# Kernel tuning notes

Measured on AMD Instinct MI355X. Metric: run time of the kernel, lower is better.

The kernel has to match this reference:

```python
import jax, jax.numpy as jnp
import numpy as np

N_QUBITS = 10
DIM = 2 ** N_QUBITS
N_TOKENS = 32
LAYERS = 2
DEGREE = 3
VOCAB = 32000
EMB = 512
N_PARAMS = 4 * N_QUBITS * LAYERS      # angles per token circuit
N_PARAMS_FF = 4 * N_QUBITS            # quantum feedforward (1 layer)
BATCH = 32


def _ry(state, wire, theta, n):
    # state: [B, 2**n] complex64; theta: [B] float32. RY = [[c,-s],[s,c]], c=cos(th/2)
    st = state.reshape(-1, 2 ** wire, 2, 2 ** (n - wire - 1))
    c = jnp.cos(theta / 2)[:, None, None]
    s = jnp.sin(theta / 2)[:, None, None]
    a, b = st[:, :, 0, :], st[:, :, 1, :]
    st = jnp.stack([c * a - s * b, s * a + c * b], axis=2)
    return st.reshape(-1, 2 ** n)


def _crx(state, ctrl, tgt, theta, n):
    # controlled-RX: apply RX=[[c,-i s],[-i s,c]] on tgt where ctrl bit == 1
    lo, hi = (ctrl, tgt) if ctrl < tgt else (tgt, ctrl)
    st = state.reshape(-1, 2 ** lo, 2, 2 ** (hi - lo - 1), 2, 2 ** (n - hi - 1))
    caxis = 2 if ctrl < tgt else 4
    taxis = 4 if ctrl < tgt else 2
    c = jnp.cos(theta / 2).reshape(-1, 1, 1, 1, 1, 1)
    s = jnp.sin(theta / 2).reshape(-1, 1, 1, 1, 1, 1)
    c0 = jax.lax.index_in_dim(st, 0, caxis, keepdims=True)
    c1 = jax.lax.index_in_dim(st, 1, caxis, keepdims=True)
    a = jax.lax.index_in_dim(c1, 0, taxis, keepdims=True)
    b = jax.lax.index_in_dim(c1, 1, taxis, keepdims=True)
    na = c * a - 1j * s * b
    nb = -1j * s * a + c * b
    c1 = jnp.concatenate([na, nb], axis=taxis)
    st = jnp.concatenate([c0, c1], axis=caxis)
    return st.reshape(-1, 2 ** n)


def _ansatz14(state, params, n, layers):
    # gate order of ansatz 14 (arXiv:1905.10876); params: [B, 4*n*layers]
    idx = 0
    for _ in range(layers):
        for i in range(n):
            state = _ry(state, i, params[:, idx], n); idx += 1
        for i in range(n - 1, -1, -1):
            state = _crx(state, i, (i + 1) % n, params[:, idx], n); idx += 1
        for i in range(n):
            state = _ry(state, i, params[:, idx], n); idx += 1
        for i in [n - 1] + list(range(n - 1)):
            state = _crx(state, i, (i - 1) % n, params[:, idx], n); idx += 1
    return state


def _measure_xyz(state, n):
    # expectation of X,Y,Z on every wire; output [B, 3*n] ordered [x..., y..., z...]
    B = state.shape[0]
    xs, ys, zs = [], [], []
    for w in range(n):
        st = state.reshape(B, 2 ** w, 2, 2 ** (n - w - 1))
        a, b = st[:, :, 0, :], st[:, :, 1, :]
        z = jnp.sum(jnp.conj(a) * b, axis=(1, 2))
        xs.append(2.0 * jnp.real(z))
        ys.append(2.0 * jnp.imag(z))
        zs.append(jnp.sum(jnp.real(a * jnp.conj(a)) - jnp.real(b * jnp.conj(b)), axis=(1, 2)))
    return jnp.stack(xs + ys + zs, axis=1)


def _forward(x, emb, w_ang, b_ang, qsvt_coeffs, lcu_re, lcu_im, qff_params, w1, b1, w2, b2):
    B, T = x.shape
    lcu = (lcu_re + 1j * lcu_im).astype(jnp.complex64)
    lcu = lcu / jnp.maximum(jnp.sum(jnp.abs(lcu)), 1e-12)          # p=1 normalize
    angles = (emb[x] @ w_ang.T + b_ang).reshape(B * T, N_PARAMS)   # [B*T, P]
    init = jnp.zeros((B, DIM), jnp.complex64).at[:, 0].set(1.0)
    acc = qsvt_coeffs[0] * init
    mono = init
    for k in range(1, DEGREE + 1):
        rep = jnp.repeat(mono, T, axis=0)                          # [B*T, D]
        st = _ansatz14(rep, angles, N_QUBITS, LAYERS).reshape(B, T, DIM)
        mono = jnp.einsum('bwi,w->bi', st, lcu)                    # LCU combine
        acc = acc + qsvt_coeffs[k] * mono
    qsvt_state = acc / jnp.sum(jnp.abs(qsvt_coeffs))
    norm = jnp.linalg.norm(qsvt_state, axis=-1, keepdims=True)
    normed = qsvt_state / jnp.maximum(norm, 1e-12)
    qff = jnp.broadcast_to(qff_params[None, :], (B, N_PARAMS_FF))
    st2 = _ansatz14(normed, qff, N_QUBITS, 1)
    ev = _measure_xyz(st2, N_QUBITS)                               # [B, 3*nq]
    h = jax.nn.relu(ev @ w1.T + b1)
    logits = h @ w2.T + b2
    return logits, jnp.mean(norm[:, 0])


def setup_inputs() -> dict:
    key = jax.random.key(0)
    ks = jax.random.split(key, 9)
    return {
        'x': jax.random.randint(ks[0], (BATCH, N_TOKENS), 0, VOCAB, dtype=jnp.int32),
        'emb': jax.random.normal(ks[1], (VOCAB, EMB), jnp.float32) * 0.02,
        'w_ang': jax.random.normal(ks[2], (N_PARAMS, EMB), jnp.float32) * (1.0 / np.sqrt(EMB)),
        'b_ang': jnp.zeros((N_PARAMS,), jnp.float32),
        'qsvt_coeffs': jax.random.uniform(ks[3], (DEGREE + 1,), jnp.float32),
        'lcu_re': jax.random.uniform(ks[4], (N_TOKENS,), jnp.float32),
        'lcu_im': jax.random.uniform(ks[5], (N_TOKENS,), jnp.float32),
        'qff_params': jax.random.uniform(ks[6], (N_PARAMS_FF,), jnp.float32),
        'w1': jax.random.normal(ks[7], (EMB, 3 * N_QUBITS), jnp.float32) * (1.0 / np.sqrt(3 * N_QUBITS)),
        'b1': jnp.zeros((EMB,), jnp.float32),
        'w2': jax.random.normal(ks[8], (VOCAB, EMB), jnp.float32) * (1.0 / np.sqrt(EMB)),
        'b2': jnp.zeros((VOCAB,), jnp.float32),
    }


def reference(x, emb, w_ang, b_ang, qsvt_coeffs, lcu_re, lcu_im, qff_params, w1, b1, w2, b2):
    return _forward(x, emb, w_ang, b_ang, qsvt_coeffs, lcu_re, lcu_im, qff_params, w1, b1, w2, b2)
```

## Files before the change

kernel.cpp:

```cpp
#include <hip/hip_runtime.h>
#include <math.h>

#define DEV __device__ __forceinline__

namespace {

struct C2 { float x, y; };

constexpr size_t OFF_CS   = 0;
constexpr size_t OFF_NRM  = 163988;
constexpr size_t OFF_MONO = 164096;
constexpr size_t OFF_ACC  = 229632;
constexpr size_t OFF_ST   = 295168;
constexpr size_t OFF_H    = 2393280;

template<int P>
DEV void ry_gate(C2 v[16], int lane, float c, float s) {
  if constexpr (P >= 6) {
    constexpr int rm = 1 << (P - 6);
#pragma unroll
    for (int r = 0; r < 16; ++r) {
      if ((r & rm) == 0) {
        C2 a = v[r], b = v[r | rm];
        v[r].x      = fmaf(c, a.x, -s * b.x);
        v[r].y      = fmaf(c, a.y, -s * b.y);
        v[r | rm].x = fmaf(s, a.x,  c * b.x);
        v[r | rm].y = fmaf(s, a.y,  c * b.y);
      }
    }
  } else {
    constexpr int lm = 1 << P;
    float sg = (lane & lm) ? s : -s;
#pragma unroll
    for (int r = 0; r < 16; ++r) {
      float px = __shfl_xor(v[r].x, lm, 64);
      float py = __shfl_xor(v[r].y, lm, 64);
      v[r].x = fmaf(c, v[r].x, sg * px);
      v[r].y = fmaf(c, v[r].y, sg * py);
    }
  }
}

template<int PC, int PT>
DEV void crx_gate(C2 v[16], int lane, float c, float s) {
  if constexpr (PT >= 6) {
    constexpr int tm = 1 << (PT - 6);
#pragma unroll
    for (int r = 0; r < 16; ++r) {
      if ((r & tm) == 0) {
        if constexpr (PC >= 6) {
          constexpr int cm = 1 << (PC - 6);
          if ((r & cm) != 0) {
            C2 a = v[r], b = v[r | tm];
            v[r].x      = fmaf(c, a.x,  s * b.y);
            v[r].y      = fmaf(c, a.y, -s * b.x);
            v[r | tm].x = fmaf(c, b.x,  s * a.y);
            v[r | tm].y = fmaf(c, b.y, -s * a.x);
          }
        } else {
          constexpr int cl = 1 << PC;
          bool ct = (lane & cl) != 0;
          C2 a = v[r], b = v[r | tm];
          float nax = fmaf(c, a.x,  s * b.y);
          float nay = fmaf(c, a.y, -s * b.x);
          float nbx = fmaf(c, b.x,  s * a.y);
          float nby = fmaf(c, b.y, -s * a.x);
          v[r].x      = ct ? nax : a.x;
          v[r].y      = ct ? nay : a.y;
          v[r | tm].x = ct ? nbx : b.x;
          v[r | tm].y = ct ? nby : b.y;
        }
      }
    }
  } else {
    constexpr int tm = 1 << PT;
#pragma unroll
    for (int r = 0; r < 16; ++r) {
      if constexpr (PC >= 6) {
        constexpr int cm = 1 << (PC - 6);
        if ((r & cm) == 0) continue;
      }
      float px = __shfl_xor(v[r].x, tm, 64);
      float py = __shfl_xor(v[r].y, tm, 64);
      float nx = fmaf(c, v[r].x,  s * py);
      float ny = fmaf(c, v[r].y, -s * px);
      if constexpr (PC >= 6) {
        v[r].x = nx; v[r].y = ny;
      } else {
        constexpr int cl = 1 << PC;
        bool ct = (lane & cl) != 0;
        v[r].x = ct ? nx : v[r].x;
        v[r].y = ct ? ny : v[r].y;
      }
    }
  }
}

#define RYG(w, g)       ry_gate<9-(w)>(v, lane, cs[2*(g)], cs[2*(g)+1])
#define CRXG(cw, tw, g) crx_gate<9-(cw), 9-(tw)>(v, lane, cs[2*(g)], cs[2*(g)+1])

DEV void apply_layer(C2 v[16], int lane, const float* __restrict__ cs) {
  RYG(0,0); RYG(1,1); RYG(2,2); RYG(3,3); RYG(4,4);
  RYG(5,5); RYG(6,6); RYG(7,7); RYG(8,8); RYG(9,9);
  CRXG(9,0,10); CRXG(8,9,11); CRXG(7,8,12); CRXG(6,7,13); CRXG(5,6,14);
  CRXG(4,5,15); CRXG(3,4,16); CRXG(2,3,17); CRXG(1,2,18); CRXG(0,1,19);
  RYG(0,20); RYG(1,21); RYG(2,22); RYG(3,23); RYG(4,24);
  RYG(5,25); RYG(6,26); RYG(7,27); RYG(8,28); RYG(9,29);
  CRXG(9,8,30); CRXG(0,9,31); CRXG(1,0,32); CRXG(2,1,33); CRXG(3,2,34);
  CRXG(4,3,35); CRXG(5,4,36); CRXG(6,5,37); CRXG(7,6,38); CRXG(8,7,39);
}

template<int P>
DEV void measure_wire(const C2 v[16], int lane, float* ev, int w) {
  float x = 0.f, y = 0.f, z = 0.f;
  if constexpr (P >= 6) {
    constexpr int rm = 1 << (P - 6);
#pragma unroll
    for (int r = 0; r < 16; ++r) {
      if ((r & rm) == 0) {
        C2 a = v[r], b = v[r | rm];
        x += a.x*b.x + a.y*b.y;
        y += a.x*b.y - a.y*b.x;
        z += (a.x*a.x + a.y*a.y) - (b.x*b.x + b.y*b.y);
      }
    }
  } else {
    constexpr int lm = 1 << P;
#pragma unroll
    for (int r = 0; r < 16; ++r) {
      float px = __shfl_xor(v[r].x, lm, 64);
      float py = __shfl_xor(v[r].y, lm, 64);
      if ((lane & lm) == 0) {
        C2 a = v[r];
        x += a.x*px + a.y*py;
        y += a.x*py - a.y*px;
        z += (a.x*a.x + a.y*a.y) - (px*px + py*py);
      }
    }
  }
  for (int s = 1; s < 64; s <<= 1) {
    x += __shfl_xor(x, s, 64);
    y += __shfl_xor(y, s, 64);
    z += __shfl_xor(z, s, 64);
  }
  if (lane == 0) {
    ev[w]      = 2.f * x;
    ev[10 + w] = 2.f * y;
    ev[20 + w] = z;
  }
}

DEV void measure_all(const C2 v[16], int lane, float* ev) {
  measure_wire<9>(v, lane, ev, 0);
  measure_wire<8>(v, lane, ev, 1);
  measure_wire<7>(v, lane, ev, 2);
  measure_wire<6>(v, lane, ev, 3);
  measure_wire<5>(v, lane, ev, 4);
  measure_wire<4>(v, lane, ev, 5);
  measure_wire<3>(v, lane, ev, 6);
  measure_wire<2>(v, lane, ev, 7);
  measure_wire<1>(v, lane, ev, 8);
  measure_wire<0>(v, lane, ev, 9);
}


template<int P>
DEV void ry8(C2 v[8], int lane, float c, float s) {
  if constexpr (P >= 6) {
    constexpr int rm = 1 << (P - 6);
#pragma unroll
    for (int r = 0; r < 8; ++r) {
      if ((r & rm) == 0) {
        C2 a = v[r], b = v[r | rm];
        v[r].x      = fmaf(c, a.x, -s * b.x);
        v[r].y      = fmaf(c, a.y, -s * b.y);
        v[r | rm].x = fmaf(s, a.x,  c * b.x);
        v[r | rm].y = fmaf(s, a.y,  c * b.y);
      }
    }
  } else {
    constexpr int lm = 1 << P;
    float sg = (lane & lm) ? s : -s;
#pragma unroll
    for (int r = 0; r < 8; ++r) {
      float px = __shfl_xor(v[r].x, lm, 64);
      float py = __shfl_xor(v[r].y, lm, 64);
      v[r].x = fmaf(c, v[r].x, sg * px);
      v[r].y = fmaf(c, v[r].y, sg * py);
    }
  }
}

template<int PT>
DEV void rx_all8(C2 v[8], int lane, float c, float s) {
  if constexpr (PT >= 6) {
    constexpr int tm = 1 << (PT - 6);
#pragma unroll
    for (int r = 0; r < 8; ++r) {
      if ((r & tm) == 0) {
        C2 a = v[r], bb = v[r | tm];
        v[r].x      = fmaf(c, a.x,  s * bb.y);
        v[r].y      = fmaf(c, a.y, -s * bb.x);
        v[r | tm].x = fmaf(c, bb.x,  s * a.y);
        v[r | tm].y = fmaf(c, bb.y, -s * a.x);
      }
    }
  } else {
    constexpr int tm = 1 << PT;
#pragma unroll
    for (int r = 0; r < 8; ++r) {
      float px = __shfl_xor(v[r].x, tm, 64);
      float py = __shfl_xor(v[r].y, tm, 64);
      v[r].x = fmaf(c, v[r].x,  s * py);
      v[r].y = fmaf(c, v[r].y, -s * px);
    }
  }
}

template<int PC, int PT>
DEV void crx8(C2 v[8], int lane, int half, float c, float s) {
  if constexpr (PC == 9) {
    if (half) rx_all8<PT>(v, lane, c, s);
  } else if constexpr (PT >= 6) {
    constexpr int tm = 1 << (PT - 6);
#pragma unroll
    for (int r = 0; r < 8; ++r) {
      if ((r & tm) == 0) {
        if constexpr (PC >= 6) {
          constexpr int cm = 1 << (PC - 6);
          if ((r & cm) != 0) {
            C2 a = v[r], bb = v[r | tm];
            v[r].x      = fmaf(c, a.x,  s * bb.y);
            v[r].y      = fmaf(c, a.y, -s * bb.x);
            v[r | tm].x = fmaf(c, bb.x,  s * a.y);
            v[r | tm].y = fmaf(c, bb.y, -s * a.x);
          }
        } else {
          constexpr int cl = 1 << PC;
          bool ct = (lane & cl) != 0;
          C2 a = v[r], bb = v[r | tm];
          float nax = fmaf(c, a.x,  s * bb.y);
          float nay = fmaf(c, a.y, -s * bb.x);
          float nbx = fmaf(c, bb.x,  s * a.y);
          float nby = fmaf(c, bb.y, -s * a.x);
          v[r].x      = ct ? nax : a.x;
          v[r].y      = ct ? nay : a.y;
          v[r | tm].x = ct ? nbx : bb.x;
          v[r | tm].y = ct ? nby : bb.y;
        }
      }
    }
  } else {
    constexpr int tm = 1 << PT;
#pragma unroll
    for (int r = 0; r < 8; ++r) {
      if constexpr (PC >= 6) {
        constexpr int cm = 1 << (PC - 6);
        if ((r & cm) == 0) continue;
      }
      float px = __shfl_xor(v[r].x, tm, 64);
      float py = __shfl_xor(v[r].y, tm, 64);
      float nx = fmaf(c, v[r].x,  s * py);
      float ny = fmaf(c, v[r].y, -s * px);
      if constexpr (PC >= 6) {
        v[r].x = nx; v[r].y = ny;
      } else {
        constexpr int cl = 1 << PC;
        bool ct = (lane & cl) != 0;
        v[r].x = ct ? nx : v[r].x;
        v[r].y = ct ? ny : v[r].y;
      }
    }
  }
}

DEV void xchg(float2 (*xb)[8][64], int wid, int lane, const C2 v[8], C2 p[8]) {
  __syncthreads();
#pragma unroll
  for (int r = 0; r < 8; ++r)
    xb[wid][r][lane] = make_float2(v[r].x, v[r].y);
  __syncthreads();
#pragma unroll
  for (int r = 0; r < 8; ++r) {
    float2 q = xb[wid ^ 1][r][lane];
    p[r].x = q.x; p[r].y = q.y;
  }
}

DEV void ry_cross(C2 v[8], const C2 p[8], int half, float c, float s) {
  float sg = half ? s : -s;
#pragma unroll
  for (int r = 0; r < 8; ++r) {
    v[r].x = fmaf(c, v[r].x, sg * p[r].x);
    v[r].y = fmaf(c, v[r].y, sg * p[r].y);
  }
}

template<int CL>
DEV void crx_cross_lane(C2 v[8], const C2 p[8], int lane, float c, float s) {
#pragma unroll
  for (int r = 0; r < 8; ++r) {
    float nx = fmaf(c, v[r].x,  s * p[r].y);
    float ny = fmaf(c, v[r].y, -s * p[r].x);
    bool ct = (lane & CL) != 0;
    v[r].x = ct ? nx : v[r].x;
    v[r].y = ct ? ny : v[r].y;
  }
}

DEV void crx_cross_reg(C2 v[8], const C2 p[8], float c, float s) {
#pragma unroll
  for (int r = 4; r < 8; ++r) {
    v[r].x = fmaf(c, v[r].x,  s * p[r].y);
    v[r].y = fmaf(c, v[r].y, -s * p[r].x);
  }
}

DEV void apply_layer_split(C2 v[8], int lane, int half, int wid,
                           const float* __restrict__ cs,
                           float2 (*xb)[8][64]) {
  C2 p[8];
  xchg(xb, wid, lane, v, p);
  ry_cross(v, p, half, cs[0], cs[1]);
  ry8<8>(v, lane, cs[2],  cs[3]);
  ry8<7>(v, lane, cs[4],  cs[5]);
  ry8<6>(v, lane, cs[6],  cs[7]);
  ry8<5>(v, lane, cs[8],  cs[9]);
  ry8<4>(v, lane, cs[10], cs[11]);
  ry8<3>(v, lane, cs[12], cs[13]);
  ry8<2>(v, lane, cs[14], cs[15]);
  ry8<1>(v, lane, cs[16], cs[17]);
  ry8<0>(v, lane, cs[18], cs[19]);
  xchg(xb, wid, lane, v, p);
  crx_cross_lane<1>(v, p, lane, cs[20], cs[21]);
  crx8<1,0>(v, lane, half, cs[22], cs[23]);
  crx8<2,1>(v, lane, half, cs[24], cs[25]);
  crx8<3,2>(v, lane, half, cs[26], cs[27]);
  crx8<4,3>(v, lane, half, cs[28], cs[29]);
  crx8<5,4>(v, lane, half, cs[30], cs[31]);
  crx8<6,5>(v, lane, half, cs[32], cs[33]);
  crx8<7,6>(v, lane, half, cs[34], cs[35]);
  crx8<8,7>(v, lane, half, cs[36], cs[37]);
  crx8<9,8>(v, lane, half, cs[38], cs[39]);
  xchg(xb, wid, lane, v, p);
  ry_cross(v, p, half, cs[40], cs[41]);
  ry8<8>(v, lane, cs[42], cs[43]);
  ry8<7>(v, lane, cs[44], cs[45]);
  ry8<6>(v, lane, cs[46], cs[47]);
  ry8<5>(v, lane, cs[48], cs[49]);
  ry8<4>(v, lane, cs[50], cs[51]);
  ry8<3>(v, lane, cs[52], cs[53]);
  ry8<2>(v, lane, cs[54], cs[55]);
  ry8<1>(v, lane, cs[56], cs[57]);
  ry8<0>(v, lane, cs[58], cs[59]);
  crx8<0,1>(v, lane, half, cs[60], cs[61]);
  crx8<9,0>(v, lane, half, cs[62], cs[63]);
  xchg(xb, wid, lane, v, p);
  crx_cross_reg(v, p, cs[64], cs[65]);
  crx8<7,8>(v, lane, half, cs[66], cs[67]);
  crx8<6,7>(v, lane, half, cs[68], cs[69]);
  crx8<5,6>(v, lane, half, cs[70], cs[71]);
  crx8<4,5>(v, lane, half, cs[72], cs[73]);
  crx8<3,4>(v, lane, half, cs[74], cs[75]);
  crx8<2,3>(v, lane, half, cs[76], cs[77]);
  crx8<1,2>(v, lane, half, cs[78], cs[79]);
}


template<int K>
__global__ __launch_bounds__(512) void k_evolve(float* __restrict__ ws,
    const float* __restrict__ lr, const float* __restrict__ li,
    const int* __restrict__ x, const float* __restrict__ emb,
    const float* __restrict__ w_ang, const float* __restrict__ b_ang) {
  __shared__ float2 xbuf[8][8][64];
  __shared__ float cs_lds[4][160];
  const int tid = threadIdx.x, g = blockIdx.x;
  const int wid = tid >> 6, lane = tid & 63;
  const int sl = wid >> 1, half = wid & 1;
  const int state = g * 4 + sl, b = state >> 5, t = state & 31;

  if constexpr (K == 1) {
    float* e4 = (float*)xbuf;
    {
      int rowi = tid >> 7, col = tid & 127;
      int row = x[g * 4 + rowi];
      ((float4*)e4)[rowi * 128 + col] =
          ((const float4*)(emb + (size_t)row * 512))[col];
    }
    __syncthreads();
    if (tid < 320) {
      int tl = tid / 80, gate = tid - tl * 80;
      const float4* wr = (const float4*)(w_ang + (size_t)gate * 512);
      const float4* ep = (const float4*)e4 + (size_t)tl * 128;
      float a = b_ang[gate];
#pragma unroll 4
      for (int j = 0; j < 128; ++j) {
        float4 w4 = wr[j], e = ep[j];
        a = fmaf(w4.x, e.x, a); a = fmaf(w4.y, e.y, a);
        a = fmaf(w4.z, e.z, a); a = fmaf(w4.w, e.w, a);
      }
      float th = 0.5f * a, cv = cosf(th), sv = sinf(th);
      cs_lds[tl][2 * gate]     = cv;
      cs_lds[tl][2 * gate + 1] = sv;
      size_t go = OFF_CS + (size_t)(g * 4 + tl) * 160 + 2 * gate;
      ws[go] = cv; ws[go + 1] = sv;
    }
    __syncthreads();
  } else {
    const float* csg = ws + OFF_CS + (size_t)g * 640;
    for (int i = tid; i < 640; i += 512) ((float*)cs_lds)[i] = csg[i];
    __syncthreads();
  }

  float lre_v = 0.f, lim_v = 0.f;
  if (lane < 32) { lre_v = lr[lane]; lim_v = li[lane]; }
  float ab = sqrtf(lre_v * lre_v + lim_v * lim_v);
  for (int s = 1; s < 64; s <<= 1) ab += __shfl_xor(ab, s, 64);
  float invL = 1.f / fmaxf(ab, 1e-12f);
  float wre = __shfl(lre_v, t, 64) * invL;
  float wim = __shfl(lim_v, t, 64) * invL;

  C2 v[8];
  if constexpr (K == 1) {
#pragma unroll
    for (int r = 0; r < 8; ++r) { v[r].x = 0.f; v[r].y = 0.f; }
    if (half == 0 && lane == 0) v[0].x = 1.f;
  } else {
    const float2* mono = (const float2*)(ws + OFF_MONO)
                       + (size_t)b * 1024 + (half << 9);
#pragma unroll
    for (int r = 0; r < 8; ++r) {
      float2 m = mono[(r << 6) | lane];
      v[r].x = m.x; v[r].y = m.y;
    }
  }

  const float* cs0 = cs_lds[sl];
  apply_layer_split(v, lane, half, wid, cs0, xbuf);
  apply_layer_split(v, lane, half, wid, cs0 + 80, xbuf);

  float2* st = (float2*)(ws + OFF_ST)
             + (size_t)state * 1024 + (half << 9);
#pragma unroll
  for (int r = 0; r < 8; ++r) {
    st[(r << 6) | lane] = make_float2(wre * v[r].x - wim * v[r].y,
                                      wre * v[r].y + wim * v[r].x);
  }
}

__global__ void k_reduce(float* __restrict__ ws, const float* __restrict__ coef, int k) {
  int idx = blockIdx.x * 256 + threadIdx.x;
  int b = idx >> 10, i = idx & 1023;
  const float2* st = (const float2*)(ws + OFF_ST) + (size_t)b * 32768 + i;
  float sx = 0.f, sy = 0.f;
#pragma unroll
  for (int t = 0; t < 32; ++t) {
    float2 vv = st[t * 1024];
    sx += vv.x; sy += vv.y;
  }
  float2* mono = (float2*)(ws + OFF_MONO);
  float2* acc  = (float2*)(ws + OFF_ACC);
  float ck = coef[k];
  if (k == 1) {
    float e0 = (i == 0) ? coef[0] : 0.f;
    acc[idx] = make_float2(fmaf(ck, sx, e0), ck * sy);
    mono[idx] = make_float2(sx, sy);
  } else {
    float2 a = acc[idx];
    a.x = fmaf(ck, sx, a.x);
    a.y = fmaf(ck, sy, a.y);
    acc[idx] = a;
    mono[idx] = make_float2(sx, sy);
  }
}

__global__ __launch_bounds__(256) void k_final(float* __restrict__ ws,
                                               const float* __restrict__ coef,
                                               const float* __restrict__ qff,
                                               const float* __restrict__ w1,
                                               const float* __restrict__ b1) {
  __shared__ float qff_lds[80];
  __shared__ float2 sv[1024];
  __shared__ float ev_lds[30];
  int tid = threadIdx.x;
  int b = blockIdx.x;
  if (tid < 40) {
    float th = 0.5f * qff[tid];
    qff_lds[2 * tid]     = cosf(th);
    qff_lds[2 * tid + 1] = sinf(th);
  }
  float den = fabsf(coef[0]) + fabsf(coef[1]) + fabsf(coef[2]) + fabsf(coef[3]);
  float invd = 1.f / den;
  float c3 = coef[3];
  const float2* stb  = (const float2*)(ws + OFF_ST) + (size_t)b * 32768;
  const float2* accb = (const float2*)(ws + OFF_ACC) + (size_t)b * 1024;
#pragma unroll
  for (int q = 0; q < 4; ++q) {
    int i = tid + q * 256;
    float sx = 0.f, sy = 0.f;
#pragma unroll
    for (int t = 0; t < 32; ++t) {
      float2 vv = stb[t * 1024 + i];
      sx += vv.x; sy += vv.y;
    }
    float2 a = accb[i];
    sv[i] = make_float2(fmaf(c3, sx, a.x) * invd, fmaf(c3, sy, a.y) * invd);
  }
  __syncthreads();
  if (tid < 64) {
    int lane = tid;
    C2 v[16];
    float ssum = 0.f;
#pragma unroll
    for (int r = 0; r < 16; ++r) {
      float2 m = sv[(r << 6) | lane];
      v[r].x = m.x; v[r].y = m.y;
      ssum += v[r].x * v[r].x + v[r].y * v[r].y;
    }
    for (int s = 1; s < 64; s <<= 1) ssum += __shfl_xor(ssum, s, 64);
    float nrm = sqrtf(ssum);
    if (lane == 0) ws[OFF_NRM + b] = nrm;
    float sc = 1.f / fmaxf(nrm, 1e-12f);
#pragma unroll
    for (int r = 0; r < 16; ++r) { v[r].x *= sc; v[r].y *= sc; }
    apply_layer(v, lane, qff_lds);
    measure_all(v, lane, ev_lds);
  }
  __syncthreads();
#pragma unroll
  for (int jj = 0; jj < 2; ++jj) {
    int j = tid + jj * 256;
    const float* wr = w1 + (size_t)j * 30;
    float a = b1[j];
#pragma unroll
    for (int q = 0; q < 30; ++q) a = fmaf(ev_lds[q], wr[q], a);
    ws[OFF_H + b * 512 + j] = fmaxf(a, 0.f);
  }
}

__global__ __launch_bounds__(256) void k_logits(const float* __restrict__ ws,
                                                const float* __restrict__ w2,
                                                const float* __restrict__ b2,
                                                float* __restrict__ out) {
  __shared__ float4 hT[4096];
  int tid = threadIdx.x;
  if (blockIdx.x == 0 && tid == 0) {
    float s = 0.f;
    for (int i = 0; i < 32; ++i) s += ws[OFF_NRM + i];
    out[32000u * 32u] = s * (1.f / 32.f);
  }
  const float4* hg = (const float4*)(ws + OFF_H);
#pragma unroll
  for (int p = 0; p < 16; ++p) {
    int idx = tid + p * 256;
    int m = idx >> 7, kf4 = idx & 127;
    hT[m * 128 + (kf4 ^ (m >> 3))] = hg[idx];
  }
  __syncthreads();

  int wv = tid >> 6, lane = tid & 63;
  int mg = lane & 3, nl = lane >> 2;
  int nbase = blockIdx.x * 64;
  float acc[4][8];
#pragma unroll
  for (int j = 0; j < 4; ++j)
#pragma unroll
    for (int mi = 0; mi < 8; ++mi) acc[j][mi] = 0.f;

  const float* wbase = w2 + (size_t)(nbase + nl * 4) * 512 + wv * 128;
  int kqb = wv * 32;
#pragma unroll 2
  for (int kf4 = 0; kf4 < 32; ++kf4) {
    int kcol = kqb + kf4;
    float4 h4[8];
#pragma unroll
    for (int mi = 0; mi < 8; ++mi) {
      int m = mg * 8 + mi;
      h4[mi] = hT[m * 128 + (kcol ^ mg)];
    }
#pragma unroll
    for (int j = 0; j < 4; ++j) {
      float4 w4 = *(const float4*)(wbase + (size_t)j * 512 + kf4 * 4);
#pragma unroll
      for (int mi = 0; mi < 8; ++mi) {
        acc[j][mi] = fmaf(w4.x, h4[mi].x, acc[j][mi]);
        acc[j][mi] = fmaf(w4.y, h4[mi].y, acc[j][mi]);
        acc[j][mi] = fmaf(w4.z, h4[mi].z, acc[j][mi]);
        acc[j][mi] = fmaf(w4.w, h4[mi].w, acc[j][mi]);
      }
    }
  }

  __syncthreads();
#pragma unroll
  for (int mi = 0; mi < 8; ++mi) {
    hT[wv * 512 + lane * 8 + (mi ^ (lane & 7))] =
        make_float4(acc[0][mi], acc[1][mi], acc[2][mi], acc[3][mi]);
  }
  __syncthreads();
  {
    int lane2 = tid & 63, grp = tid >> 6;
    int mg2 = lane2 & 3, nl2 = lane2 >> 2;
#pragma unroll
    for (int jj = 0; jj < 2; ++jj) {
      int mi2 = grp * 2 + jj;
      float4 s0 = hT[0 * 512 + lane2 * 8 + (mi2 ^ (lane2 & 7))];
      float4 s1 = hT[1 * 512 + lane2 * 8 + (mi2 ^ (lane2 & 7))];
      float4 s2 = hT[2 * 512 + lane2 * 8 + (mi2 ^ (lane2 & 7))];
      float4 s3 = hT[3 * 512 + lane2 * 8 + (mi2 ^ (lane2 & 7))];
      float sx = s0.x + s1.x + s2.x + s3.x;
      float sy = s0.y + s1.y + s2.y + s3.y;
      float sz = s0.z + s1.z + s2.z + s3.z;
      float sw = s0.w + s1.w + s2.w + s3.w;
      int m = mg2 * 8 + mi2;
      int col = nbase + nl2 * 4;
      float4 b2v = *(const float4*)(b2 + col);
      float4 res = make_float4(sx + b2v.x, sy + b2v.y, sz + b2v.z, sw + b2v.w);
      *(float4*)(out + (size_t)m * 32000 + col) = res;
    }
  }
}

}

extern "C" void kernel_launch(void* const* d_in, const int* in_sizes, int n_in,
                              void* d_out, int out_size, void* d_ws, size_t ws_size,
                              hipStream_t stream) {
  (void)in_sizes; (void)n_in; (void)out_size; (void)ws_size;
  const int*   x    = (const int*)d_in[0];
  const float* emb  = (const float*)d_in[1];
  const float* wang = (const float*)d_in[2];
  const float* bang = (const float*)d_in[3];
  const float* coef = (const float*)d_in[4];
  const float* lre  = (const float*)d_in[5];
  const float* lim  = (const float*)d_in[6];
  const float* qff  = (const float*)d_in[7];
  const float* w1   = (const float*)d_in[8];
  const float* b1   = (const float*)d_in[9];
  const float* w2   = (const float*)d_in[10];
  const float* b2   = (const float*)d_in[11];
  float* out = (float*)d_out;
  float* ws  = (float*)d_ws;

  hipLaunchKernelGGL(k_evolve<1>, dim3(256), dim3(512), 0, stream,
                     ws, lre, lim, x, emb, wang, bang);
  hipLaunchKernelGGL(k_reduce, dim3(128), dim3(256), 0, stream, ws, coef, 1);
  hipLaunchKernelGGL(k_evolve<2>, dim3(256), dim3(512), 0, stream,
                     ws, lre, lim, x, emb, wang, bang);
  hipLaunchKernelGGL(k_reduce, dim3(128), dim3(256), 0, stream, ws, coef, 2);
  hipLaunchKernelGGL(k_evolve<3>, dim3(256), dim3(512), 0, stream,
                     ws, lre, lim, x, emb, wang, bang);
  hipLaunchKernelGGL(k_final,  dim3(32),  dim3(256), 0, stream, ws, coef, qff, w1, b1);
  hipLaunchKernelGGL(k_logits, dim3(500), dim3(256), 0, stream, ws, w2, b2, out);
}
```

Measured before the change: 153.8 us.

## Use one state per block with double-buffered LDS exchange, halving barriers

```diff
diff --git a/kernel.cpp b/kernel.cpp
--- a/kernel.cpp
+++ b/kernel.cpp
@@ -274,15 +274,14 @@
   }
 }
 
-DEV void xchg(float2 (*xb)[8][64], int wid, int lane, const C2 v[8], C2 p[8]) {
+DEV void xchg1(float2 (*xb)[8][64], int half, int lane, const C2 v[8], C2 p[8]) {
+#pragma unroll
+  for (int r = 0; r < 8; ++r)
+    xb[half][r][lane] = make_float2(v[r].x, v[r].y);
   __syncthreads();
 #pragma unroll
-  for (int r = 0; r < 8; ++r)
-    xb[wid][r][lane] = make_float2(v[r].x, v[r].y);
-  __syncthreads();
-#pragma unroll
   for (int r = 0; r < 8; ++r) {
-    float2 q = xb[wid ^ 1][r][lane];
+    float2 q = xb[half ^ 1][r][lane];
     p[r].x = q.x; p[r].y = q.y;
   }
 }
@@ -316,11 +315,11 @@
   }
 }
 
-DEV void apply_layer_split(C2 v[8], int lane, int half, int wid,
+DEV void apply_layer_split(C2 v[8], int lane, int half,
                            const float* __restrict__ cs,
-                           float2 (*xb)[8][64]) {
+                           float2 (*xbA)[8][64], float2 (*xbB)[8][64]) {
   C2 p[8];
-  xchg(xb, wid, lane, v, p);
+  xchg1(xbA, half, lane, v, p);
   ry_cross(v, p, half, cs[0], cs[1]);
   ry8<8>(v, lane, cs[2],  cs[3]);
   ry8<7>(v, lane, cs[4],  cs[5]);
@@ -331,7 +330,7 @@
   ry8<2>(v, lane, cs[14], cs[15]);
   ry8<1>(v, lane, cs[16], cs[17]);
   ry8<0>(v, lane, cs[18], cs[19]);
-  xchg(xb, wid, lane, v, p);
+  xchg1(xbB, half, lane, v, p);
   crx_cross_lane<1>(v, p, lane, cs[20], cs[21]);
   crx8<1,0>(v, lane, half, cs[22], cs[23]);
   crx8<2,1>(v, lane, half, cs[24], cs[25]);
@@ -342,7 +341,7 @@
   crx8<7,6>(v, lane, half, cs[34], cs[35]);
   crx8<8,7>(v, lane, half, cs[36], cs[37]);
   crx8<9,8>(v, lane, half, cs[38], cs[39]);
-  xchg(xb, wid, lane, v, p);
+  xchg1(xbA, half, lane, v, p);
   ry_cross(v, p, half, cs[40], cs[41]);
   ry8<8>(v, lane, cs[42], cs[43]);
   ry8<7>(v, lane, cs[44], cs[45]);
@@ -355,7 +354,7 @@
   ry8<0>(v, lane, cs[58], cs[59]);
   crx8<0,1>(v, lane, half, cs[60], cs[61]);
   crx8<9,0>(v, lane, half, cs[62], cs[63]);
-  xchg(xb, wid, lane, v, p);
+  xchg1(xbB, half, lane, v, p);
   crx_cross_reg(v, p, cs[64], cs[65]);
   crx8<7,8>(v, lane, half, cs[66], cs[67]);
   crx8<6,7>(v, lane, half, cs[68], cs[69]);
@@ -368,31 +367,28 @@
 
 
 template<int K>
-__global__ __launch_bounds__(512) void k_evolve(float* __restrict__ ws,
+__global__ __launch_bounds__(128) void k_evolve(float* __restrict__ ws,
     const float* __restrict__ lr, const float* __restrict__ li,
     const int* __restrict__ x, const float* __restrict__ emb,
     const float* __restrict__ w_ang, const float* __restrict__ b_ang) {
-  __shared__ float2 xbuf[8][8][64];
-  __shared__ float cs_lds[4][160];
+  __shared__ float2 xbufA[2][8][64];
+  __shared__ float2 xbufB[2][8][64];
+  __shared__ float cs_lds[160];
   const int tid = threadIdx.x, g = blockIdx.x;
-  const int wid = tid >> 6, lane = tid & 63;
-  const int sl = wid >> 1, half = wid & 1;
-  const int state = g * 4 + sl, b = state >> 5, t = state & 31;
+  const int half = tid >> 6, lane = tid & 63;
+  const int b = g >> 5, t = g & 31;
 
   if constexpr (K == 1) {
-    float* e4 = (float*)xbuf;
+    float* e4 = (float*)xbufA;
     {
-      int rowi = tid >> 7, col = tid & 127;
-      int row = x[g * 4 + rowi];
-      ((float4*)e4)[rowi * 128 + col] =
-          ((const float4*)(emb + (size_t)row * 512))[col];
+      int row = x[g];
+      ((float4*)e4)[tid] = ((const float4*)(emb + (size_t)row * 512))[tid];
     }
     __syncthreads();
-    if (tid < 320) {
-      int tl = tid / 80, gate = tid - tl * 80;
-      const float4* wr = (const float4*)(w_ang + (size_t)gate * 512);
-      const float4* ep = (const float4*)e4 + (size_t)tl * 128;
-      float a = b_ang[gate];
+    if (tid < 80) {
+      const float4* wr = (const float4*)(w_ang + (size_t)tid * 512);
+      const float4* ep = (const float4*)e4;
+      float a = b_ang[tid];
 #pragma unroll 4
       for (int j = 0; j < 128; ++j) {
         float4 w4 = wr[j], e = ep[j];
@@ -400,15 +396,15 @@
         a = fmaf(w4.z, e.z, a); a = fmaf(w4.w, e.w, a);
       }
       float th = 0.5f * a, cv = cosf(th), sv = sinf(th);
-      cs_lds[tl][2 * gate]     = cv;
-      cs_lds[tl][2 * gate + 1] = sv;
-      size_t go = OFF_CS + (size_t)(g * 4 + tl) * 160 + 2 * gate;
+      cs_lds[2 * tid]     = cv;
+      cs_lds[2 * tid + 1] = sv;
+      size_t go = OFF_CS + (size_t)g * 160 + 2 * tid;
       ws[go] = cv; ws[go + 1] = sv;
     }
     __syncthreads();
   } else {
-    const float* csg = ws + OFF_CS + (size_t)g * 640;
-    for (int i = tid; i < 640; i += 512) ((float*)cs_lds)[i] = csg[i];
+    const float* csg = ws + OFF_CS + (size_t)g * 160;
+    for (int i = tid; i < 160; i += 128) cs_lds[i] = csg[i];
     __syncthreads();
   }
 
@@ -435,12 +431,10 @@
     }
   }
 
-  const float* cs0 = cs_lds[sl];
-  apply_layer_split(v, lane, half, wid, cs0, xbuf);
-  apply_layer_split(v, lane, half, wid, cs0 + 80, xbuf);
-
-  float2* st = (float2*)(ws + OFF_ST)
-             + (size_t)state * 1024 + (half << 9);
+  apply_layer_split(v, lane, half, cs_lds, xbufA, xbufB);
+  apply_layer_split(v, lane, half, cs_lds + 80, xbufA, xbufB);
+
+  float2* st = (float2*)(ws + OFF_ST) + (size_t)g * 1024 + (half << 9);
 #pragma unroll
   for (int r = 0; r < 8; ++r) {
     st[(r << 6) | lane] = make_float2(wre * v[r].x - wim * v[r].y,
@@ -642,13 +636,13 @@
   float* out = (float*)d_out;
   float* ws  = (float*)d_ws;
 
-  hipLaunchKernelGGL(k_evolve<1>, dim3(256), dim3(512), 0, stream,
+  hipLaunchKernelGGL(k_evolve<1>, dim3(1024), dim3(128), 0, stream,
                      ws, lre, lim, x, emb, wang, bang);
   hipLaunchKernelGGL(k_reduce, dim3(128), dim3(256), 0, stream, ws, coef, 1);
-  hipLaunchKernelGGL(k_evolve<2>, dim3(256), dim3(512), 0, stream,
+  hipLaunchKernelGGL(k_evolve<2>, dim3(1024), dim3(128), 0, stream,
                      ws, lre, lim, x, emb, wang, bang);
   hipLaunchKernelGGL(k_reduce, dim3(128), dim3(256), 0, stream, ws, coef, 2);
-  hipLaunchKernelGGL(k_evolve<3>, dim3(256), dim3(512), 0, stream,
+  hipLaunchKernelGGL(k_evolve<3>, dim3(1024), dim3(128), 0, stream,
                      ws, lre, lim, x, emb, wang, bang);
   hipLaunchKernelGGL(k_final,  dim3(32),  dim3(256), 0, stream, ws, coef, qff, w1, b1);
   hipLaunchKernelGGL(k_logits, dim3(500), dim3(256), 0, stream, ws, w2, b2, out);
```

Measured after the change: 152.7 us. No clear change (-0.7%).
